# Kernel optimization log

Measured on AMD Instinct MI355X. Metric: run time of the kernel, lower is better.

The kernel has to match this reference:

```python
import jax, jax.numpy as jnp
import numpy as np

BUF = 16  # max polygon vertex buffer (convex 9-gon clipped by 4 half-planes -> <= 13 verts)


def _shoelace(V, c):
    # area of polygon stored in buffer V[:c]
    i = jnp.arange(V.shape[0])
    nxt = jnp.where(i + 1 < c, i + 1, 0)
    Vn = V[nxt]
    contrib = jnp.where(i < c, V[:, 0] * Vn[:, 1] - Vn[:, 0] * V[:, 1], 0.0)
    return 0.5 * jnp.abs(contrib.sum())


def _convex_hull(P):
    # exact convex hull of n small points; returns CCW-ordered vertex buffer [BUF,2] and count
    n = P.shape[0]
    d = P[None, :, :] - P[:, None, :]  # p_j - p_i
    minc = jnp.full((n, n), jnp.inf, P.dtype)
    for k in range(n):  # fixed small loop, keeps memory at [n,n]
        w = (P[k] - P)[:, None, :]
        minc = jnp.minimum(minc, d[..., 0] * w[..., 1] - d[..., 1] * w[..., 0])
    minc = jax.lax.stop_gradient(minc)  # hull membership is discrete
    edge = (minc >= -1e-6) & (~jnp.eye(n, dtype=bool))  # (i,j) is CCW hull edge iff all pts left
    hull = edge.any(1)
    cnt = hull.sum()
    cen = (P * hull[:, None]).sum(0) / jnp.maximum(cnt, 1)
    ang = jnp.arctan2(P[:, 1] - cen[1], P[:, 0] - cen[0])
    keyv = jnp.where(hull, jax.lax.stop_gradient(ang), jnp.inf)
    order = jnp.argsort(keyv)
    V = jnp.zeros((BUF, 2), P.dtype).at[:n].set(P[order])
    return V, cnt


def _clip(V, c, a, b):
    # Sutherland-Hodgman clip of convex polygon (V,c) by half-plane left of a->b
    i = jnp.arange(BUF)
    active = i < c
    nxt = jnp.where(i + 1 < c, i + 1, 0)
    nx = V[nxt]
    e = b - a
    s_cur = e[0] * (V[:, 1] - a[1]) - e[1] * (V[:, 0] - a[0])
    s_nxt = e[0] * (nx[:, 1] - a[1]) - e[1] * (nx[:, 0] - a[0])
    in_cur = s_cur >= 0
    in_nxt = s_nxt >= 0
    den = s_cur - s_nxt
    safe = jnp.abs(den) > 1e-9
    t = jnp.where(safe, s_cur / jnp.where(safe, den, 1.0), 0.0)
    ipt = V + t[:, None] * (nx - V)
    f_int = active & (in_cur != in_nxt)
    f_nxt = active & in_nxt
    pts = jnp.stack([ipt, nx], 1).reshape(2 * BUF, 2)
    flg = jnp.stack([f_int, f_nxt], 1).reshape(2 * BUF)
    pos = jnp.cumsum(flg) - 1
    idx = jnp.where(flg, pos, BUF)  # invalid slots dropped
    out = jnp.zeros((BUF, 2), V.dtype).at[idx].set(pts, mode='drop')
    return out, flg.sum()


def _order_ccw(Q):
    cen = Q.mean(0)
    ang = jnp.arctan2(Q[:, 1] - cen[1], Q[:, 0] - cen[0])
    return Q[jnp.argsort(jax.lax.stop_gradient(ang))]


def _per_point(gt4, p9):
    # giou_loss + out_of_box loss for one (gt quad, 9 pred points) pair
    gt = _order_ccw(gt4)
    Vp, cp = _convex_hull(p9)          # predicted convex polygon (OrientedRepPoints convex hull)
    a_pred = _shoelace(Vp, cp)
    a_gt = _shoelace(jnp.zeros((BUF, 2), gt.dtype).at[:4].set(gt), 4)
    V, c = Vp, cp
    for e in range(4):
        V, c = _clip(V, c, gt[e], gt[(e + 1) % 4])
    a_int = _shoelace(V, c)
    union = a_pred + a_gt - a_int
    iou = a_int / (union + 1e-16)
    Vh, ch = _convex_hull(jnp.concatenate([gt4, p9], 0))  # hull of all 13 points
    a_hull = _shoelace(Vh, ch)
    giou = iou - (a_hull - union) / (a_hull + 1e-16)
    # out-of-box distance: positive distance of pred points outside the gt quad edges
    b = jnp.roll(gt, -1, 0)
    e2 = b - gt
    rel = p9[:, None, :] - gt[None, :, :]
    s = (e2[None, :, 0] * rel[..., 1] - e2[None, :, 1] * rel[..., 0]) / (jnp.linalg.norm(e2, axis=1)[None, :] + 1e-9)
    oob = jax.nn.relu((-s).max(1)).mean()
    return 1.0 - giou, oob


def _assign(points_xy, points_lvl, gt_obb):
    # OBBPointAssigner: sequential per-GT closest-point assignment (pos_num=1, scale=4)
    xs = gt_obb[:, 0::2]
    ys = gt_obb[:, 1::2]
    xmin, xmax = xs.min(1), xs.max(1)
    ymin, ymax = ys.min(1), ys.max(1)
    cxy = jnp.stack([(xmin + xmax) / 2, (ymin + ymax) / 2], 1)
    wh = jnp.maximum(jnp.stack([xmax - xmin, ymax - ymin], 1), 1e-6)
    lvl_min, lvl_max = points_lvl.min(), points_lvl.max()
    glvl = jnp.clip(((jnp.log2(wh[:, 0] / 4.0) + jnp.log2(wh[:, 1] / 4.0)) / 2).astype(jnp.int32), lvl_min, lvl_max)
    K = gt_obb.shape[0]
    Np = points_xy.shape[0]

    def body(carry, g):
        inds, dist = carry
        c_xy, c_wh, c_lvl, gi = g
        dmask = points_lvl == c_lvl
        dd = jnp.linalg.norm((points_xy - c_xy) / c_wh, axis=1)
        dd = jnp.where(dmask, dd, jnp.inf)
        j = jnp.argmin(dd)
        md = dd[j]
        better = md < dist[j]
        inds = inds.at[j].set(jnp.where(better, gi + 1, inds[j]))
        dist = dist.at[j].set(jnp.where(better, md, dist[j]))
        return (inds, dist), None

    init = (jnp.zeros(Np, jnp.int32), jnp.full(Np, jnp.inf, points_xy.dtype))
    (inds, _), _ = jax.lax.scan(body, init, (cxy, wh, glvl, jnp.arange(K, dtype=jnp.int32)))
    return inds


def _stage(rep, inds, labels, gt_obb):
    posm = (labels > 0).astype(rep.dtype)
    gidx = jnp.maximum(inds - 1, 0)
    gt4 = gt_obb[gidx].reshape(-1, 4, 2)
    p9 = rep.reshape(-1, 9, 2)
    gl, oob = jax.vmap(_per_point)(gt4, p9)
    npos = jnp.maximum(posm.sum(), 1.0)
    return (gl * posm).sum() / npos, (oob * posm).sum() / npos


def _forward(rpi, rpr, cls, stride, gob, glab):
    stride = jax.lax.stop_gradient(stride)
    plvl = jnp.log2(stride).astype(jnp.int32)
    inds_i = _assign(jax.lax.stop_gradient(rpi[:, 8:10]), plvl, jax.lax.stop_gradient(gob))
    inds_r = _assign(jax.lax.stop_gradient(rpr[:, 8:10]), plvl, jax.lax.stop_gradient(gob))
    lab_i = jnp.where(inds_i > 0, glab[jnp.maximum(inds_i - 1, 0)], 0)
    lab_r = jnp.where(inds_r > 0, glab[jnp.maximum(inds_r - 1, 0)], 0)
    loc_i, sc_i = _stage(rpi, inds_i, lab_i, gob)
    loc_r, sc_r = _stage(rpr, inds_r, lab_r, gob)
    logp = jax.nn.log_softmax(cls, -1)
    cls_loss = -jnp.take_along_axis(logp, lab_r[:, None], 1).mean()
    return 1.0 * cls_loss + 0.3 * loc_i + 1.0 * loc_r + 0.05 * sc_i + 0.1 * sc_r


def setup_inputs() -> dict:
    key = jax.random.key(0)
    ks = jax.random.split(key, 8)
    strides = [8, 16, 32, 64, 128]
    batch = 2
    centers_list, stride_list = [], []
    for s in strides:
        hw = 1536 // s
        c = (jnp.arange(hw, dtype=jnp.float32) + 0.5) * s
        gx, gy = jnp.meshgrid(c, c, indexing='ij')
        cen = jnp.stack([gx.reshape(-1), gy.reshape(-1)], 1)
        cen = jnp.tile(cen, (batch, 1))
        centers_list.append(cen)
        stride_list.append(jnp.full((cen.shape[0],), float(s), jnp.float32))
    centers = jnp.concatenate(centers_list, 0)
    points_stride = jnp.concatenate(stride_list, 0)
    N = centers.shape[0]  # 98208
    base = jnp.tile(centers[:, None, :], (1, 9, 1)).reshape(N, 18)
    scale18 = jnp.repeat(points_stride[:, None], 18, 1)
    rpi = base + jax.random.normal(ks[0], (N, 18), jnp.float32) * scale18 * 1.5
    rpr = base + jax.random.normal(ks[1], (N, 18), jnp.float32) * scale18 * 1.0
    classification = jax.random.normal(ks[2], (N, 16), jnp.float32)
    K = 64
    cx = jax.random.uniform(ks[3], (K,), minval=128.0, maxval=1408.0)
    cy = jax.random.uniform(ks[4], (K,), minval=128.0, maxval=1408.0)
    w = jax.random.uniform(ks[5], (K,), minval=48.0, maxval=400.0)
    h = jax.random.uniform(ks[6], (K,), minval=48.0, maxval=400.0)
    th = jax.random.uniform(ks[7], (K,), minval=0.0, maxval=float(np.pi))
    ct, st = jnp.cos(th), jnp.sin(th)
    dx = jnp.stack([-w, w, w, -w], 1) / 2
    dy = jnp.stack([-h, -h, h, h], 1) / 2
    xs = cx[:, None] + dx * ct[:, None] - dy * st[:, None]
    ys = cy[:, None] + dx * st[:, None] + dy * ct[:, None]
    gt_obboxes = jnp.stack([xs, ys], 2).reshape(K, 8)
    gt_labels = jax.random.randint(jax.random.fold_in(key, 7), (K,), 1, 16)
    return {"rep_points_init": rpi, "rep_points_refine": rpr, "classification": classification,
            "points_stride": points_stride, "gt_obboxes": gt_obboxes, "gt_labels": gt_labels}


def reference(rep_points_init, rep_points_refine, classification, points_stride, gt_obboxes, gt_labels):
    return _forward(rep_points_init, rep_points_refine, classification, points_stride, gt_obboxes, gt_labels)
```

## Files before the change

kernel.cpp:

```cpp
#include <hip/hip_runtime.h>
#include <math.h>
#include <stdint.h>

#pragma clang fp contract(off)

#define SUB 16

struct WS {
  double sums[8];
  unsigned long long packed[128];
  int lo[8], hi[8];
  float gcx[64], gcy[64], gw[64], gh[64];
  int glvl[64];
  unsigned cntpub[2];
  unsigned done2;
};

__global__ void k_pre(const float* __restrict__ stridev, const float* __restrict__ gob,
                      int N, int K, WS* ws) {
  __shared__ int bnd[9];
  __shared__ int slmin, slmax;
  int t = threadIdx.x;
  if (t < 8) ws->sums[t] = 0.0;
  if (t < 128) ws->packed[t] = ~0ULL;
  if (t == 0) { ws->done2 = 0u; ws->cntpub[0] = 0u; ws->cntpub[1] = 0u; }
  if (t < 9) {
    float v = (float)(1 << t);
    int lo = 0, hi = N;
    while (lo < hi) { int mid = (lo + hi) >> 1; if (stridev[mid] < v) lo = mid + 1; else hi = mid; }
    bnd[t] = lo;
  }
  __syncthreads();
  if (t == 0) {
    int a = 7, b = 0;
    for (int l = 0; l < 8; l++) {
      int lo = bnd[l], hi = bnd[l + 1];
      ws->lo[l] = lo; ws->hi[l] = hi;
      if (hi > lo) { if (l < a) a = l; if (l > b) b = l; }
    }
    slmin = a; slmax = b;
  }
  __syncthreads();
  if (t < K && t < 64) {
    const float* g = gob + t * 8;
    float x0 = g[0], x1 = g[2], x2 = g[4], x3 = g[6];
    float y0 = g[1], y1 = g[3], y2 = g[5], y3 = g[7];
    float xmin = fminf(fminf(x0, x1), fminf(x2, x3));
    float xmax = fmaxf(fmaxf(x0, x1), fmaxf(x2, x3));
    float ymin = fminf(fminf(y0, y1), fminf(y2, y3));
    float ymax = fmaxf(fmaxf(y0, y1), fmaxf(y2, y3));
    float w = fmaxf(xmax - xmin, 1e-6f);
    float h = fmaxf(ymax - ymin, 1e-6f);
    ws->gcx[t] = (xmin + xmax) * 0.5f;
    ws->gcy[t] = (ymin + ymax) * 0.5f;
    ws->gw[t] = w; ws->gh[t] = h;
    int gl = (int)((log2f(w * 0.25f) + log2f(h * 0.25f)) * 0.5f);
    gl = gl < slmin ? slmin : (gl > slmax ? slmax : gl);
    ws->glvl[t] = gl;
  }
}

__global__ void __launch_bounds__(256) k_main(const float* __restrict__ rpi,
                                              const float* __restrict__ rpr,
                                              const float* __restrict__ cls,
                                              int N, int K, int AB, WS* ws) {
  __shared__ unsigned long long sb[256];
  int t = threadIdx.x;
  int b = blockIdx.x;
  if (b < AB) {
    int s = b % SUB;
    int ak = b / SUB;
    int a = ak / K;
    int k = ak % K;
    int L = ws->glvl[k];
    int lo = ws->lo[L], hi = ws->hi[L];
    float cx = ws->gcx[k], cy = ws->gcy[k], w = ws->gw[k], h = ws->gh[k];
    const float* rep = a ? rpr : rpi;
    unsigned long long best = ~0ULL;
    for (int i = lo + s * 256 + t; i < hi; i += SUB * 256) {
      const float2 p = *(const float2*)(rep + (size_t)i * 18 + 8);
      float dx = (p.x - cx) / w, dy = (p.y - cy) / h;
      float dd = sqrtf(dx * dx + dy * dy);
      unsigned long long pk = ((unsigned long long)__float_as_uint(dd) << 32) | (unsigned)i;
      if (pk < best) best = pk;
    }
    sb[t] = best;
    __syncthreads();
    for (int off = 128; off > 0; off >>= 1) {
      if (t < off) { unsigned long long o = sb[t + off]; if (o < sb[t]) sb[t] = o; }
      __syncthreads();
    }
    if (t == 0) atomicMin(&ws->packed[a * 64 + k], sb[0]);
  } else {
    int i = (b - AB) * 256 + t;
    double v = 0.0;
    if (i < N) {
      const float4* r = (const float4*)(cls + (size_t)i * 16);
      float4 q0 = r[0], q1 = r[1], q2 = r[2], q3 = r[3];
      float x[16] = {q0.x, q0.y, q0.z, q0.w, q1.x, q1.y, q1.z, q1.w,
                     q2.x, q2.y, q2.z, q2.w, q3.x, q3.y, q3.z, q3.w};
      float m = x[0];
      for (int j = 1; j < 16; j++) m = fmaxf(m, x[j]);
      float ssum = 0.f;
      for (int j = 0; j < 16; j++) ssum += expf(x[j] - m);
      v = (double)(logf(ssum) + m - x[0]);
    }
    double* sd = (double*)sb;
    sd[t] = v;
    __syncthreads();
    for (int off = 128; off > 0; off >>= 1) {
      if (t < off) sd[t] += sd[t + off];
      __syncthreads();
    }
    if (t == 0) atomicAdd(&ws->sums[0], sd[0]);
  }
}


__device__ __forceinline__ float shoe(const float* VX, const float* VY, int c) {
  float s = 0.f;
  #pragma unroll
  for (int i = 0; i < 16; i++) {
    if (i < c) {
      int nx = (i + 1 < c) ? ((i + 1 < 16) ? i + 1 : 15) : 0;
      s += VX[i] * VY[nx] - VX[nx] * VY[i];
    }
  }
  return 0.5f * fabsf(s);
}

__device__ __forceinline__ int clip_edge(const float* SX, const float* SY, float* DX, float* DY,
                                         int c, float ax, float ay, float bx, float by, int lane) {
  if (lane < 16) { DX[lane] = 0.f; DY[lane] = 0.f; }
  bool f_int = false, f_nxt = false;
  float ix = 0.f, iy = 0.f, nxv = 0.f, nyv = 0.f;
  if (lane < 16 && lane < c) {
    int nxt = (lane + 1 < c) ? lane + 1 : 0;
    if (nxt > 15) nxt = 15;
    float cxv = SX[lane], cyv = SY[lane];
    nxv = SX[nxt]; nyv = SY[nxt];
    float ex = bx - ax, ey = by - ay;
    float s_cur = ex * (cyv - ay) - ey * (cxv - ax);
    float s_nxt = ex * (nyv - ay) - ey * (nxv - ax);
    bool in_cur = s_cur >= 0.f, in_nxt = s_nxt >= 0.f;
    float den = s_cur - s_nxt;
    bool safe = fabsf(den) > 1e-9f;
    float tt = safe ? s_cur / den : 0.f;
    ix = cxv + tt * (nxv - cxv);
    iy = cyv + tt * (nyv - cyv);
    f_int = (in_cur != in_nxt);
    f_nxt = in_nxt;
  }
  unsigned long long bi = __ballot(f_int), bn = __ballot(f_nxt);
  unsigned long long lt = (1ULL << lane) - 1ULL;
  int below = __popcll(bi & lt) + __popcll(bn & lt);
  if (f_int && below < 16) { DX[below] = ix; DY[below] = iy; }
  int posn = below + (f_int ? 1 : 0);
  if (f_nxt && posn < 16) { DX[posn] = nxv; DY[posn] = nyv; }
  __syncthreads();
  return __popcll(bi) + __popcll(bn);
}

template <int NP>
__device__ __forceinline__ int hull_wave(const float* PX, const float* PY, int base,
                                         float* VX, float* VY, float* KEY, int lane) {
  constexpr int TOT = NP * NP;
  unsigned long long B0 = 0, B1 = 0, B2 = 0;
  {
    bool h = false;
    int idx = lane;
    if (idx < TOT) {
      int i = idx / NP, j = idx % NP;
      if (i != j) {
        float pix = PX[base + i], piy = PY[base + i];
        float dx = PX[base + j] - pix, dy = PY[base + j] - piy;
        float m = INFINITY;
        #pragma unroll
        for (int k = 0; k < NP; k++)
          m = fminf(m, dx * (PY[base + k] - piy) - dy * (PX[base + k] - pix));
        h = (m >= -1e-6f);
      }
    }
    B0 = __ballot(h);
  }
  if constexpr (TOT > 64) {
    bool h = false;
    int idx = lane + 64;
    if (idx < TOT) {
      int i = idx / NP, j = idx % NP;
      if (i != j) {
        float pix = PX[base + i], piy = PY[base + i];
        float dx = PX[base + j] - pix, dy = PY[base + j] - piy;
        float m = INFINITY;
        #pragma unroll
        for (int k = 0; k < NP; k++)
          m = fminf(m, dx * (PY[base + k] - piy) - dy * (PX[base + k] - pix));
        h = (m >= -1e-6f);
      }
    }
    B1 = __ballot(h);
  }
  if constexpr (TOT > 128) {
    bool h = false;
    int idx = lane + 128;
    if (idx < TOT) {
      int i = idx / NP, j = idx % NP;
      if (i != j) {
        float pix = PX[base + i], piy = PY[base + i];
        float dx = PX[base + j] - pix, dy = PY[base + j] - piy;
        float m = INFINITY;
        #pragma unroll
        for (int k = 0; k < NP; k++)
          m = fminf(m, dx * (PY[base + k] - piy) - dy * (PX[base + k] - pix));
        h = (m >= -1e-6f);
      }
    }
    B2 = __ballot(h);
  }
  bool hull_i = false;
  if (lane < NP) {
    int s = lane * NP, w = s >> 6, off = s & 63;
    unsigned long long Bw = (w == 0) ? B0 : ((w == 1) ? B1 : B2);
    unsigned long long Bw1 = (w == 0) ? B1 : ((w == 1) ? B2 : 0ULL);
    unsigned long long bits = Bw >> off;
    if (off) bits |= Bw1 << (64 - off);
    hull_i = (bits & ((1ULL << NP) - 1ULL)) != 0ULL;
  }
  unsigned long long hmask = __ballot(hull_i);
  int cnt = __popcll(hmask);
  float cx = 0.f, cy = 0.f;
  #pragma unroll
  for (int k = 0; k < NP; k++)
    if ((hmask >> k) & 1ULL) { cx += PX[base + k]; cy += PY[base + k]; }
  float dn = (float)(cnt > 1 ? cnt : 1);
  cx /= dn; cy /= dn;
  if (lane < NP)
    KEY[lane] = hull_i ? atan2f(PY[base + lane] - cy, PX[base + lane] - cx) : INFINITY;
  if (lane < 16) { VX[lane] = 0.f; VY[lane] = 0.f; }
  __syncthreads();
  if (lane < NP) {
    float ki = KEY[lane];
    int r = 0;
    #pragma unroll
    for (int j2 = 0; j2 < NP; j2++) {
      float kj = KEY[j2];
      r += (int)((kj < ki) || (kj == ki && j2 < lane));
    }
    VX[r] = PX[base + lane];
    VY[r] = PY[base + lane];
  }
  __syncthreads();
  return cnt;
}

__global__ void __launch_bounds__(64) k_post(const float* __restrict__ rpi,
                                             const float* __restrict__ rpr,
                                             const float* __restrict__ gob,
                                             const int* __restrict__ glab,
                                             const float* __restrict__ cls,
                                             int N, float* out, WS* ws) {
  __shared__ float PXs[16], PYs[16], VX[16], VY[16], DX[16], DY[16], KEY[16], RED[9];
  __shared__ int SJ[64];
  __shared__ unsigned long long SMK[64];
  int lane = threadIdx.x;
  int b = blockIdx.x;
  int a = b >> 6, p = b & 63;

  unsigned long long pk = ws->packed[a * 64 + lane];
  bool valid = (pk != ~0ULL);
  SJ[lane] = valid ? (int)(unsigned)(pk & 0xffffffffu) : (-1 - lane);
  SMK[lane] = (pk & 0xffffffff00000000ULL) | (unsigned)lane;
  __syncthreads();
  bool win = false;
  if (valid) {
    int j = SJ[lane];
    unsigned long long me = SMK[lane];
    win = true;
    for (int o = 0; o < 64; o++)
      if (SJ[o] == j && SMK[o] < me) win = false;
  }
  unsigned long long wmask = __ballot(win);
  int cnt = __popcll(wmask);
  if (p == 0 && lane == 0) atomicExch(&ws->cntpub[a], (unsigned)cnt);

  bool active = (p < cnt);
  if (active) {
    int kk = 0;
    { int c2 = 0;
      for (int o = 0; o < 64; o++)
        if ((wmask >> o) & 1ULL) { if (c2 == p) { kk = o; break; } c2++; } }
    int j = SJ[kk];
    const float* rep = (a ? rpr : rpi) + (size_t)j * 18;
    const float* gt8 = gob + (size_t)kk * 8;
    if (lane < 4) { PXs[lane] = gt8[2 * lane]; PYs[lane] = gt8[2 * lane + 1]; }
    else if (lane < 13) { int q = lane - 4; PXs[lane] = rep[2 * q]; PYs[lane] = rep[2 * q + 1]; }
    __syncthreads();

    float cenx = (((PXs[0] + PXs[1]) + PXs[2]) + PXs[3]) / 4.f;
    float ceny = (((PYs[0] + PYs[1]) + PYs[2]) + PYs[3]) / 4.f;
    float angv[4];
    int r4[4];
    #pragma unroll
    for (int i = 0; i < 4; i++) angv[i] = atan2f(PYs[i] - ceny, PXs[i] - cenx);
    #pragma unroll
    for (int i = 0; i < 4; i++) {
      int r = 0;
      #pragma unroll
      for (int j2 = 0; j2 < 4; j2++)
        r += (int)((angv[j2] < angv[i]) || (angv[j2] == angv[i] && j2 < i));
      r4[i] = r;
    }
    float qx[4], qy[4];
    #pragma unroll
    for (int d = 0; d < 4; d++) {
      float sx = 0.f, sy = 0.f;
      #pragma unroll
      for (int i = 0; i < 4; i++) if (r4[i] == d) { sx = PXs[i]; sy = PYs[i]; }
      qx[d] = sx; qy[d] = sy;
    }

    int cp = hull_wave<9>(PXs, PYs, 4, VX, VY, KEY, lane);
    float a_pred = shoe(VX, VY, cp);

    float sgt = 0.f;
    #pragma unroll
    for (int i = 0; i < 4; i++) {
      int nx = (i + 1) & 3;
      sgt += qx[i] * qy[nx] - qx[nx] * qy[i];
    }
    float a_gt = 0.5f * fabsf(sgt);

    int c = cp;
    c = clip_edge(VX, VY, DX, DY, c, qx[0], qy[0], qx[1], qy[1], lane);
    c = clip_edge(DX, DY, VX, VY, c, qx[1], qy[1], qx[2], qy[2], lane);
    c = clip_edge(VX, VY, DX, DY, c, qx[2], qy[2], qx[3], qy[3], lane);
    c = clip_edge(DX, DY, VX, VY, c, qx[3], qy[3], qx[0], qy[0], lane);
    float a_int = shoe(VX, VY, c);

    float uni = a_pred + a_gt - a_int;
    float iou = a_int / (uni + 1e-16f);

    int ch = hull_wave<13>(PXs, PYs, 0, VX, VY, KEY, lane);
    float a_hull = shoe(VX, VY, ch);
    float giou = iou - (a_hull - uni) / (a_hull + 1e-16f);
    float gl = 1.f - giou;

    float mxv = -INFINITY;
    if (lane < 36) {
      int pp = lane >> 2, e = lane & 3;
      float ax = e == 0 ? qx[0] : e == 1 ? qx[1] : e == 2 ? qx[2] : qx[3];
      float ay = e == 0 ? qy[0] : e == 1 ? qy[1] : e == 2 ? qy[2] : qy[3];
      float bx2 = e == 0 ? qx[1] : e == 1 ? qx[2] : e == 2 ? qx[3] : qx[0];
      float by2 = e == 0 ? qy[1] : e == 1 ? qy[2] : e == 2 ? qy[3] : qy[0];
      float ex = bx2 - ax, ey = by2 - ay;
      float nrm = sqrtf(ex * ex + ey * ey) + 1e-9f;
      float px = PXs[4 + pp], py = PYs[4 + pp];
      float s = (ex * (py - ay) - ey * (px - ax)) / nrm;
      mxv = -s;
    }
    float o1 = __shfl_xor(mxv, 1); mxv = fmaxf(mxv, o1);
    float o2 = __shfl_xor(mxv, 2); mxv = fmaxf(mxv, o2);
    if (lane < 36 && (lane & 3) == 0) RED[lane >> 2] = fmaxf(mxv, 0.f);
    __syncthreads();
    if (lane == 0) {
      float acc = 0.f;
      #pragma unroll
      for (int pp = 0; pp < 9; pp++) acc += RED[pp];
      float oob = acc / 9.f;
      atomicAdd(&ws->sums[1 + a * 2], (double)gl);
      atomicAdd(&ws->sums[2 + a * 2], (double)oob);
      if (a == 1) {
        int lab = glab[kk];
        double corr = (double)cls[(size_t)j * 16] - (double)cls[(size_t)j * 16 + lab];
        atomicAdd(&ws->sums[0], corr);
      }
    }
  }

  __syncthreads();
  if (lane == 0) {
    __threadfence();
    unsigned d = atomicAdd(&ws->done2, 1u);
    if (d == gridDim.x - 1) {
      __threadfence();
      double s0 = atomicAdd(&ws->sums[0], 0.0);
      double s1 = atomicAdd(&ws->sums[1], 0.0);
      double s2 = atomicAdd(&ws->sums[2], 0.0);
      double s3 = atomicAdd(&ws->sums[3], 0.0);
      double s4 = atomicAdd(&ws->sums[4], 0.0);
      unsigned c0 = atomicAdd(&ws->cntpub[0], 0u);
      unsigned c1 = atomicAdd(&ws->cntpub[1], 0u);
      double n0 = (double)(c0 > 1u ? c0 : 1u);
      double n1 = (double)(c1 > 1u ? c1 : 1u);
      out[0] = (float)(s0 / (double)N + 0.3 * (s1 / n0) + 1.0 * (s3 / n1) +
                       0.05 * (s2 / n0) + 0.1 * (s4 / n1));
    }
  }
}

extern "C" void kernel_launch(void* const* d_in, const int* in_sizes, int n_in,
                              void* d_out, int out_size, void* d_ws, size_t ws_size,
                              hipStream_t stream) {
  const float* rpi = (const float*)d_in[0];
  const float* rpr = (const float*)d_in[1];
  const float* cls = (const float*)d_in[2];
  const float* pstride = (const float*)d_in[3];
  const float* gob = (const float*)d_in[4];
  const int* glab = (const int*)d_in[5];
  int N = in_sizes[3];
  int K = in_sizes[5];
  if (K > 64) K = 64;
  WS* ws = (WS*)d_ws;

  int AB = 2 * K * SUB;
  int nb = (N + 255) / 256;
  k_pre<<<1, 256, 0, stream>>>(pstride, gob, N, K, ws);
  k_main<<<AB + nb, 256, 0, stream>>>(rpi, rpr, cls, N, K, AB, ws);
  k_post<<<128, 64, 0, stream>>>(rpi, rpr, gob, glab, cls, N, (float*)d_out, ws);
}
```

Baseline: 104.4 us.

## Fuse gt preprocessing into point-parallel main kernel with per-wave argmin reduction

Replaces the per-ground-truth block scan over each pyramid level's point range with a point-parallel scheme. Each thread loads its init and refine points once, derives its level from log2 of its stride, loops over all GT boxes with ballot skipping, and reduces the argmin with wave shuffles and a small shared-memory merge. GT box centres and inverse sizes are now computed per block in shared memory, so the prep kernel's binary searches are dropped. It also compares squared distances instead of taking sqrt and multiplies by reciprocals instead of dividing, which assumes sorted power-of-two strides and can change rounding or tie-breaking.

```diff
diff --git a/kernel.cpp b/kernel.cpp
--- a/kernel.cpp
+++ b/kernel.cpp
@@ -4,44 +4,34 @@
 
 #pragma clang fp contract(off)
 
-#define SUB 16
-
 struct WS {
   double sums[8];
   unsigned long long packed[128];
-  int lo[8], hi[8];
-  float gcx[64], gcy[64], gw[64], gh[64];
-  int glvl[64];
   unsigned cntpub[2];
   unsigned done2;
 };
 
-__global__ void k_pre(const float* __restrict__ stridev, const float* __restrict__ gob,
-                      int N, int K, WS* ws) {
-  __shared__ int bnd[9];
-  __shared__ int slmin, slmax;
+__global__ void k_init(WS* ws) {
   int t = threadIdx.x;
   if (t < 8) ws->sums[t] = 0.0;
   if (t < 128) ws->packed[t] = ~0ULL;
   if (t == 0) { ws->done2 = 0u; ws->cntpub[0] = 0u; ws->cntpub[1] = 0u; }
-  if (t < 9) {
-    float v = (float)(1 << t);
-    int lo = 0, hi = N;
-    while (lo < hi) { int mid = (lo + hi) >> 1; if (stridev[mid] < v) lo = mid + 1; else hi = mid; }
-    bnd[t] = lo;
-  }
-  __syncthreads();
-  if (t == 0) {
-    int a = 7, b = 0;
-    for (int l = 0; l < 8; l++) {
-      int lo = bnd[l], hi = bnd[l + 1];
-      ws->lo[l] = lo; ws->hi[l] = hi;
-      if (hi > lo) { if (l < a) a = l; if (l > b) b = l; }
-    }
-    slmin = a; slmax = b;
-  }
-  __syncthreads();
-  if (t < K && t < 64) {
+}
+
+__global__ void __launch_bounds__(256) k_main(const float* __restrict__ rpi,
+                                              const float* __restrict__ rpr,
+                                              const float* __restrict__ cls,
+                                              const float* __restrict__ stridev,
+                                              const float* __restrict__ gob,
+                                              int N, int K, WS* ws) {
+  __shared__ float gcx[64], gcy[64], giw[64], gih[64];
+  __shared__ int glv[64];
+  __shared__ unsigned long long wmin[4][128];
+  __shared__ double sd[256];
+  int t = threadIdx.x;
+  int i = blockIdx.x * 256 + t;
+
+  if (t < K) {
     const float* g = gob + t * 8;
     float x0 = g[0], x1 = g[2], x2 = g[4], x3 = g[6];
     float y0 = g[1], y1 = g[3], y2 = g[5], y3 = g[7];
@@ -51,69 +41,83 @@
     float ymax = fmaxf(fmaxf(y0, y1), fmaxf(y2, y3));
     float w = fmaxf(xmax - xmin, 1e-6f);
     float h = fmaxf(ymax - ymin, 1e-6f);
-    ws->gcx[t] = (xmin + xmax) * 0.5f;
-    ws->gcy[t] = (ymin + ymax) * 0.5f;
-    ws->gw[t] = w; ws->gh[t] = h;
+    gcx[t] = (xmin + xmax) * 0.5f;
+    gcy[t] = (ymin + ymax) * 0.5f;
+    giw[t] = 1.f / w;
+    gih[t] = 1.f / h;
+    int lmin = (int)log2f(stridev[0]);
+    int lmax = (int)log2f(stridev[N - 1]);
     int gl = (int)((log2f(w * 0.25f) + log2f(h * 0.25f)) * 0.5f);
-    gl = gl < slmin ? slmin : (gl > slmax ? slmax : gl);
-    ws->glvl[t] = gl;
-  }
-}
-
-__global__ void __launch_bounds__(256) k_main(const float* __restrict__ rpi,
-                                              const float* __restrict__ rpr,
-                                              const float* __restrict__ cls,
-                                              int N, int K, int AB, WS* ws) {
-  __shared__ unsigned long long sb[256];
-  int t = threadIdx.x;
-  int b = blockIdx.x;
-  if (b < AB) {
-    int s = b % SUB;
-    int ak = b / SUB;
-    int a = ak / K;
-    int k = ak % K;
-    int L = ws->glvl[k];
-    int lo = ws->lo[L], hi = ws->hi[L];
-    float cx = ws->gcx[k], cy = ws->gcy[k], w = ws->gw[k], h = ws->gh[k];
-    const float* rep = a ? rpr : rpi;
-    unsigned long long best = ~0ULL;
-    for (int i = lo + s * 256 + t; i < hi; i += SUB * 256) {
-      const float2 p = *(const float2*)(rep + (size_t)i * 18 + 8);
-      float dx = (p.x - cx) / w, dy = (p.y - cy) / h;
-      float dd = sqrtf(dx * dx + dy * dy);
-      unsigned long long pk = ((unsigned long long)__float_as_uint(dd) << 32) | (unsigned)i;
-      if (pk < best) best = pk;
-    }
-    sb[t] = best;
+    gl = gl < lmin ? lmin : (gl > lmax ? lmax : gl);
+    glv[t] = gl;
+  }
+  unsigned long long* wf = &wmin[0][0];
+  wf[t] = ~0ULL;
+  wf[t + 256] = ~0ULL;
+
+  bool act = (i < N);
+  int L = -1;
+  float xi = 0.f, yi = 0.f, xr = 0.f, yr = 0.f;
+  if (act) {
+    L = (int)log2f(stridev[i]);
+    const float2 pi = *(const float2*)(rpi + (size_t)i * 18 + 8);
+    const float2 pr = *(const float2*)(rpr + (size_t)i * 18 + 8);
+    xi = pi.x; yi = pi.y; xr = pr.x; yr = pr.y;
+  }
+  __syncthreads();
+
+  int lane = t & 63, wv = t >> 6;
+  for (int k = 0; k < K; k++) {
+    bool m = act && (glv[k] == L);
+    if (__ballot(m)) {
+      unsigned long long p0 = ~0ULL, p1 = ~0ULL;
+      if (m) {
+        float cx = gcx[k], cy = gcy[k], iw = giw[k], ih = gih[k];
+        float dx = (xi - cx) * iw, dy = (yi - cy) * ih;
+        float d2 = dx * dx + dy * dy;
+        p0 = ((unsigned long long)__float_as_uint(d2) << 32) | (unsigned)i;
+        dx = (xr - cx) * iw; dy = (yr - cy) * ih;
+        d2 = dx * dx + dy * dy;
+        p1 = ((unsigned long long)__float_as_uint(d2) << 32) | (unsigned)i;
+      }
+      #pragma unroll
+      for (int off = 32; off > 0; off >>= 1) {
+        unsigned long long o0 = __shfl_xor(p0, off);
+        unsigned long long o1 = __shfl_xor(p1, off);
+        if (o0 < p0) p0 = o0;
+        if (o1 < p1) p1 = o1;
+      }
+      if (lane == 0) { wmin[wv][k] = p0; wmin[wv][64 + k] = p1; }
+    }
+  }
+  __syncthreads();
+  if (t < 128) {
+    unsigned long long v = wmin[0][t];
+    if (wmin[1][t] < v) v = wmin[1][t];
+    if (wmin[2][t] < v) v = wmin[2][t];
+    if (wmin[3][t] < v) v = wmin[3][t];
+    if (v != ~0ULL) atomicMin(&ws->packed[t], v);
+  }
+
+  double v = 0.0;
+  if (act) {
+    const float4* r = (const float4*)(cls + (size_t)i * 16);
+    float4 q0 = r[0], q1 = r[1], q2 = r[2], q3 = r[3];
+    float x[16] = {q0.x, q0.y, q0.z, q0.w, q1.x, q1.y, q1.z, q1.w,
+                   q2.x, q2.y, q2.z, q2.w, q3.x, q3.y, q3.z, q3.w};
+    float m = x[0];
+    for (int j = 1; j < 16; j++) m = fmaxf(m, x[j]);
+    float ssum = 0.f;
+    for (int j = 0; j < 16; j++) ssum += expf(x[j] - m);
+    v = (double)(logf(ssum) + m - x[0]);
+  }
+  sd[t] = v;
+  __syncthreads();
+  for (int off = 128; off > 0; off >>= 1) {
+    if (t < off) sd[t] += sd[t + off];
     __syncthreads();
-    for (int off = 128; off > 0; off >>= 1) {
-      if (t < off) { unsigned long long o = sb[t + off]; if (o < sb[t]) sb[t] = o; }
-      __syncthreads();
-    }
-    if (t == 0) atomicMin(&ws->packed[a * 64 + k], sb[0]);
-  } else {
-    int i = (b - AB) * 256 + t;
-    double v = 0.0;
-    if (i < N) {
-      const float4* r = (const float4*)(cls + (size_t)i * 16);
-      float4 q0 = r[0], q1 = r[1], q2 = r[2], q3 = r[3];
-      float x[16] = {q0.x, q0.y, q0.z, q0.w, q1.x, q1.y, q1.z, q1.w,
-                     q2.x, q2.y, q2.z, q2.w, q3.x, q3.y, q3.z, q3.w};
-      float m = x[0];
-      for (int j = 1; j < 16; j++) m = fmaxf(m, x[j]);
-      float ssum = 0.f;
-      for (int j = 0; j < 16; j++) ssum += expf(x[j] - m);
-      v = (double)(logf(ssum) + m - x[0]);
-    }
-    double* sd = (double*)sb;
-    sd[t] = v;
-    __syncthreads();
-    for (int off = 128; off > 0; off >>= 1) {
-      if (t < off) sd[t] += sd[t + off];
-      __syncthreads();
-    }
-    if (t == 0) atomicAdd(&ws->sums[0], sd[0]);
-  }
+  }
+  if (t == 0) atomicAdd(&ws->sums[0], sd[0]);
 }
 
 
@@ -412,9 +416,8 @@
   if (K > 64) K = 64;
   WS* ws = (WS*)d_ws;
 
-  int AB = 2 * K * SUB;
   int nb = (N + 255) / 256;
-  k_pre<<<1, 256, 0, stream>>>(pstride, gob, N, K, ws);
-  k_main<<<AB + nb, 256, 0, stream>>>(rpi, rpr, cls, N, K, AB, ws);
+  k_init<<<1, 256, 0, stream>>>(ws);
+  k_main<<<nb, 256, 0, stream>>>(rpi, rpr, cls, pstride, gob, N, K, ws);
   k_post<<<128, 64, 0, stream>>>(rpi, rpr, gob, glab, cls, N, (float*)d_out, ws);
 }
```

Result: slower. 122.4 us (+17.2%).
